# Performance work log

Hardware: AMD Instinct MI355X
Metric: run time of the kernel (lower is better)

The kernel has to match this reference:

```python
import jax, jax.numpy as jnp
import numpy as np
import math


def _align_seq_len(e, target_n):
    # e: (B, H, N_enc, hd) -> (B, H, target_n, hd) via bilinear resize on sqrt grid
    B, H, N_enc, D = e.shape
    if N_enc == target_n:
        return e
    h_e = int(math.sqrt(N_enc))
    h_t = int(math.sqrt(target_n))
    img = jnp.transpose(e, (0, 1, 3, 2)).reshape(B, H, D, h_e, h_e)
    img = jax.image.resize(img, (B, H, D, h_t, h_t), method='bilinear')
    return jnp.transpose(img.reshape(B, H, D, target_n), (0, 1, 3, 2))


def setup_inputs() -> dict:
    key = jax.random.key(0)
    ks = jax.random.split(key, 7)
    B, N, D, H = 4, 1024, 1152, 16
    hd = D // H
    N_enc = 1024
    s_in = 1.0 / math.sqrt(D)
    return {
        'x': jax.random.normal(ks[0], (B, N, D), jnp.float32),
        'enc_k': jax.random.normal(ks[1], (B, H, N_enc, hd), jnp.float32),
        'enc_v': jax.random.normal(ks[2], (B, H, N_enc, hd), jnp.float32),
        'qkv_w': jax.random.normal(ks[3], (3 * D, D), jnp.float32) * s_in,
        'qkv_b': jax.random.normal(ks[4], (3 * D,), jnp.float32) * 0.02,
        'proj_w': jax.random.normal(ks[5], (D, D), jnp.float32) * s_in,
        'proj_b': jax.random.normal(ks[6], (D,), jnp.float32) * 0.02,
        'stage': 2,
    }


def reference(x, enc_k, enc_v, qkv_w, qkv_b, proj_w, proj_b, stage):
    B, N, C = x.shape
    H = enc_k.shape[1]
    hd = C // H
    scale = hd ** (-0.5)

    qkv = (x @ qkv_w.T + qkv_b).reshape(B, N, 3, H, hd)
    qkv = jnp.transpose(qkv, (2, 0, 3, 1, 4))  # (3, B, H, N, hd)
    q, k, v = qkv[0], qkv[1], qkv[2]

    distill_loss = jnp.float32(0.0)
    if stage == 1:
        ek = _align_seq_len(enc_k, N)
        ev = _align_seq_len(enc_v, N)
        attn = jax.nn.softmax(jnp.einsum('bhnd,bhmd->bhnm', q * scale, ek), axis=-1)
        x_out = jnp.einsum('bhnm,bhmd->bhnd', attn, ev)
    elif stage == 2:
        ek = _align_seq_len(enc_k, N)
        ev = _align_seq_len(enc_v, N)
        attn_own = jax.nn.softmax(jnp.einsum('bhnd,bhmd->bhnm', q * scale, k), axis=-1)
        x_out = jnp.einsum('bhnm,bhmd->bhnd', attn_own, v)
        qd = jax.lax.stop_gradient(q)
        attn_enc = jax.nn.softmax(jnp.einsum('bhnd,bhmd->bhnm', qd * scale, ek), axis=-1)
        o_star = jax.lax.stop_gradient(jnp.einsum('bhnm,bhmd->bhnd', attn_enc, ev))
        distill_loss = jnp.mean((x_out - o_star) ** 2)
    else:
        attn = jax.nn.softmax(jnp.einsum('bhnd,bhmd->bhnm', q * scale, k), axis=-1)
        x_out = jnp.einsum('bhnm,bhmd->bhnd', attn, v)

    x_out = jnp.transpose(x_out, (0, 2, 1, 3)).reshape(B, N, C)
    out = x_out @ proj_w.T + proj_b
    return out, distill_loss
```

## Files before the change

### kernel.cpp

```cpp
#include <hip/hip_runtime.h>
#include <hip/hip_bf16.h>

#define PB 4
#define PN 1024
#define PC 1152
#define PH 16
#define PHD 72
#define BH 64
#define QKV_COLS 3456
#define OUT_ELEMS ((size_t)PB*PN*PC)
#define K_DIM 1152

#define CHUNK_HALVES 6144
#define HEAD_HALVES (16*CHUNK_HALVES)
#define BUF_HALVES ((size_t)BH*HEAD_HALVES)

typedef _Float16 half8_t __attribute__((ext_vector_type(8)));
typedef _Float16 half4_t __attribute__((ext_vector_type(4)));
typedef float float4v __attribute__((ext_vector_type(4)));

__device__ __forceinline__ void load16_lds(const _Float16* g, _Float16* l) {
    __builtin_amdgcn_global_load_lds(
        (const __attribute__((address_space(1))) void*)g,
        (__attribute__((address_space(3))) void*)l, 16, 0, 0);
}

__global__ __launch_bounds__(256) void f32_to_f16(
    const float* __restrict__ in, _Float16* __restrict__ out, int n8)
{
    int i = blockIdx.x * 256 + threadIdx.x;
    if (i >= n8) return;
    float4 a = ((const float4*)in)[2 * i];
    float4 b = ((const float4*)in)[2 * i + 1];
    half8_t h;
    h[0] = (_Float16)a.x; h[1] = (_Float16)a.y; h[2] = (_Float16)a.z; h[3] = (_Float16)a.w;
    h[4] = (_Float16)b.x; h[5] = (_Float16)b.y; h[6] = (_Float16)b.z; h[7] = (_Float16)b.w;
    ((half8_t*)out)[i] = h;
}

__global__ __launch_bounds__(256) void zero_qpad(_Float16* __restrict__ qh)
{
    int i = blockIdx.x * 256 + threadIdx.x;
    int chunk = i / 192, within = i - chunk * 192;
    half8_t z = {};
    *(half8_t*)(qh + (size_t)chunk * CHUNK_HALVES + 4608 + within * 8) = z;
}

__global__ __launch_bounds__(256) void enc_convert(
    const float* __restrict__ ek, const float* __restrict__ ev,
    _Float16* __restrict__ ekh, _Float16* __restrict__ evth)
{
    const int bh = blockIdx.y, nblk = blockIdx.x, t = threadIdx.x;
    const float* ksrc = ek + ((size_t)bh * PN + nblk * 64) * PHD;
    const float* vsrc = ev + ((size_t)bh * PN + nblk * 64) * PHD;
    _Float16* kdst = ekh  + ((size_t)bh * 16 + nblk) * CHUNK_HALVES;
    _Float16* vdst = evth + ((size_t)bh * 16 + nblk) * CHUNK_HALVES;
    for (int i = t; i < 64 * 18; i += 256) {
        int n = i / 18, d4 = (i % 18) * 4;
        float4 kv = *(const float4*)&ksrc[n * PHD + d4];
        float4 vv = *(const float4*)&vsrc[n * PHD + d4];
        float ka[4] = {kv.x, kv.y, kv.z, kv.w};
        float va[4] = {vv.x, vv.y, vv.z, vv.w};
#pragma unroll
        for (int kk = 0; kk < 4; ++kk) {
            int d = d4 + kk;
            kdst[(d >> 3) * 512 + n * 8 + (d & 7)] = (_Float16)ka[kk];
            vdst[(n >> 3) * 768 + d * 8 + (n & 7)] = (_Float16)va[kk];
        }
    }
}

template<int MODE>
__global__ __launch_bounds__(256) void gemm_mfma(
    const _Float16* __restrict__ A, const _Float16* __restrict__ Bm,
    const float* __restrict__ bias,
    _Float16* __restrict__ qh, _Float16* __restrict__ kh,
    _Float16* __restrict__ vth, float* __restrict__ out, int c_tiles)
{
    const int t    = threadIdx.x;
    const int lane = t & 63;
    const int w    = t >> 6;
    const int wm   = w >> 1, wn = w & 1;
    const int lrow = lane & 15, quad = lane >> 4;

    const int per_group = c_tiles * 8;
    const int g  = blockIdx.x / per_group;
    const int r_ = blockIdx.x - g * per_group;
    const int m0 = (g * 8 + (r_ & 7)) * 128;
    const int c0 = (r_ >> 3) * 128;

    __shared__ _Float16 As[8192];
    __shared__ _Float16 Bs[8192];

    int rowS[4], koff[4], ldsOff[4];
#pragma unroll
    for (int i = 0; i < 4; ++i) {
        int idx = w * 256 + i * 64 + lane;
        int kt2 = idx >> 9, qq = (idx >> 7) & 3;
        rowS[i]   = idx & 127;
        koff[i]   = kt2 * 32 + qq * 8;
        ldsOff[i] = idx * 8;
    }

    const _Float16* aBase = A  + (size_t)m0 * K_DIM;
    const _Float16* bBase = Bm + (size_t)c0 * K_DIM;

    float4v acc[4][4];
#pragma unroll
    for (int ti = 0; ti < 4; ++ti)
#pragma unroll
        for (int tj = 0; tj < 4; ++tj)
            acc[ti][tj] = (float4v){0.f, 0.f, 0.f, 0.f};

    for (int kb = 0; kb < K_DIM; kb += 64) {
        __syncthreads();
#pragma unroll
        for (int i = 0; i < 4; ++i) {
            load16_lds(aBase + (size_t)rowS[i] * K_DIM + kb + koff[i], &As[ldsOff[i]]);
            load16_lds(bBase + (size_t)rowS[i] * K_DIM + kb + koff[i], &Bs[ldsOff[i]]);
        }
        __syncthreads();
#pragma unroll
        for (int s = 0; s < 2; ++s) {
            half8_t af[4], bf[4];
#pragma unroll
            for (int ti = 0; ti < 4; ++ti)
                af[ti] = *(const half8_t*)&As[(((s * 4 + quad) * 128) + wm * 64 + ti * 16 + lrow) * 8];
#pragma unroll
            for (int tj = 0; tj < 4; ++tj)
                bf[tj] = *(const half8_t*)&Bs[(((s * 4 + quad) * 128) + wn * 64 + tj * 16 + lrow) * 8];
#pragma unroll
            for (int ti = 0; ti < 4; ++ti)
#pragma unroll
                for (int tj = 0; tj < 4; ++tj)
                    acc[ti][tj] = __builtin_amdgcn_mfma_f32_16x16x32_f16(
                        af[ti], bf[tj], acc[ti][tj], 0, 0, 0);
        }
    }

    if (MODE == 0) {
        const float scale = 0.11785113019775792f;
#pragma unroll
        for (int tj = 0; tj < 4; ++tj) {
            int c = c0 + wn * 64 + tj * 16 + lrow;
            float bv = bias[c];
            int jq  = c / PC;
            int rem = c - jq * PC;
            int h   = rem / PHD;
            int d   = rem - h * PHD;
#pragma unroll
            for (int ti = 0; ti < 4; ++ti)
#pragma unroll
                for (int r = 0; r < 4; ++r) {
                    int m = m0 + wm * 64 + ti * 16 + quad * 4 + r;
                    int b = m >> 10, n = m & 1023;
                    int bh = b * PH + h;
                    size_t chunk = ((size_t)bh * 16 + (n >> 6)) * CHUNK_HALVES;
                    float val = acc[ti][tj][r] + bv;
                    if (jq == 0)
                        qh[chunk + (d >> 3) * 512 + (n & 63) * 8 + (d & 7)] = (_Float16)(val * scale);
                    else if (jq == 1)
                        kh[chunk + (d >> 3) * 512 + (n & 63) * 8 + (d & 7)] = (_Float16)val;
                    else
                        vth[chunk + ((n & 63) >> 3) * 768 + d * 8 + (n & 7)] = (_Float16)val;
                }
        }
    } else {
#pragma unroll
        for (int tj = 0; tj < 4; ++tj) {
            int c = c0 + wn * 64 + tj * 16 + lrow;
            float bv = bias[c];
#pragma unroll
            for (int ti = 0; ti < 4; ++ti)
#pragma unroll
                for (int r = 0; r < 4; ++r) {
                    int m = m0 + wm * 64 + ti * 16 + quad * 4 + r;
                    out[(size_t)m * PC + c] = acc[ti][tj][r] + bv;
                }
        }
    }
}

__device__ __forceinline__ void attn_step(
    const _Float16* Qs, const _Float16* Ks, const _Float16* Vts, _Float16* Pw,
    float4v* O, float& m_run, float& l_run, int w, int ln, int quad)
{
    float4v accS[4];
#pragma unroll
    for (int ct = 0; ct < 4; ++ct) accS[ct] = (float4v){0.f, 0.f, 0.f, 0.f};
#pragma unroll
    for (int ks = 0; ks < 3; ++ks) {
        half8_t qf = *(const half8_t*)&Qs[(((ks * 4 + quad) * 64) + w * 16 + ln) * 8];
#pragma unroll
        for (int ct = 0; ct < 4; ++ct) {
            half8_t kf = *(const half8_t*)&Ks[(((ks * 4 + quad) * 64) + ct * 16 + ln) * 8];
            accS[ct] = __builtin_amdgcn_mfma_f32_16x16x32_f16(kf, qf, accS[ct], 0, 0, 0);
        }
    }

    float mx = -1e30f;
#pragma unroll
    for (int ct = 0; ct < 4; ++ct)
#pragma unroll
        for (int r = 0; r < 4; ++r) mx = fmaxf(mx, accS[ct][r]);
    mx = fmaxf(mx, __shfl_xor(mx, 16));
    mx = fmaxf(mx, __shfl_xor(mx, 32));
    float m_new = fmaxf(m_run, mx);
    float alpha = __expf(m_run - m_new);
    m_run = m_new;

    float lsum = 0.f;
    const int pbase = (quad >> 1) * 128 + ln * 8 + (quad & 1) * 4;
#pragma unroll
    for (int ct = 0; ct < 4; ++ct) {
        half4_t pk;
#pragma unroll
        for (int r = 0; r < 4; ++r) {
            float p = __expf(accS[ct][r] - m_new);
            lsum += p;
            pk[r] = (_Float16)p;
        }
        *(half4_t*)&Pw[pbase + ct * 256] = pk;
    }
    lsum += __shfl_xor(lsum, 16);
    lsum += __shfl_xor(lsum, 32);
    l_run = l_run * alpha + lsum;

#pragma unroll
    for (int ct = 0; ct < 5; ++ct) O[ct] *= alpha;

#pragma unroll
    for (int ks = 0; ks < 2; ++ks) {
        half8_t pf = *(const half8_t*)&Pw[(ks * 4 + quad) * 128 + ln * 8];
#pragma unroll
        for (int ct = 0; ct < 5; ++ct) {
            half8_t vf = *(const half8_t*)&Vts[(((ks * 4 + quad) * 96) + ct * 16 + ln) * 8];
            O[ct] = __builtin_amdgcn_mfma_f32_16x16x32_f16(vf, pf, O[ct], 0, 0, 0);
        }
    }
}

__global__ __launch_bounds__(256) void attn_fused(
    const _Float16* __restrict__ qh, const _Float16* __restrict__ kh,
    const _Float16* __restrict__ vth,
    const _Float16* __restrict__ ekh, const _Float16* __restrict__ evth,
    _Float16* __restrict__ xouth, float* __restrict__ loss_out)
{
    const int t = threadIdx.x;
    const int lane = t & 63;
    const int w = t >> 6;
    const int ln = lane & 15;
    const int quad = lane >> 4;

    const int lid  = blockIdx.x;
    const int bh   = (lid & 7) * 8 + ((lid >> 3) >> 4);
    const int nblk = (lid >> 3) & 15;

    __shared__ _Float16 Qs[CHUNK_HALVES];
    __shared__ _Float16 KsA[CHUNK_HALVES];
    __shared__ _Float16 VsA[CHUNK_HALVES];
    __shared__ _Float16 KsB[CHUNK_HALVES];
    __shared__ _Float16 VsB[CHUNK_HALVES];
    __shared__ _Float16 Ps[4096];
    __shared__ float red[256];

    _Float16* Pw = Ps + w * 1024;

    const _Float16* qc = qh + ((size_t)bh * 16 + nblk) * CHUNK_HALVES;
    const _Float16* kbo = kh   + (size_t)bh * HEAD_HALVES;
    const _Float16* vbo = vth  + (size_t)bh * HEAD_HALVES;
    const _Float16* kbe = ekh  + (size_t)bh * HEAD_HALVES;
    const _Float16* vbe = evth + (size_t)bh * HEAD_HALVES;

#pragma unroll
    for (int i = 0; i < 3; ++i) {
        int u = i * 256 + t;
        load16_lds(qc + u * 8, &Qs[u * 8]);
        load16_lds(kbo + u * 8, &KsA[u * 8]);
        load16_lds(vbo + u * 8, &VsA[u * 8]);
    }
    __syncthreads();

    float4v Oo[5], Oe[5];
#pragma unroll
    for (int ct = 0; ct < 5; ++ct) {
        Oo[ct] = (float4v){0.f, 0.f, 0.f, 0.f};
        Oe[ct] = (float4v){0.f, 0.f, 0.f, 0.f};
    }
    float m_o = -1e30f, l_o = 0.f;
    float m_e = -1e30f, l_e = 0.f;

    for (int kt = 0; kt < 16; ++kt) {
        {
            const _Float16* kc = kbe + (size_t)kt * CHUNK_HALVES;
            const _Float16* vc = vbe + (size_t)kt * CHUNK_HALVES;
#pragma unroll
            for (int i = 0; i < 3; ++i) {
                int u = i * 256 + t;
                load16_lds(kc + u * 8, &KsB[u * 8]);
                load16_lds(vc + u * 8, &VsB[u * 8]);
            }
        }
        attn_step(Qs, KsA, VsA, Pw, Oo, m_o, l_o, w, ln, quad);
        __syncthreads();

        if (kt < 15) {
            const _Float16* kc = kbo + (size_t)(kt + 1) * CHUNK_HALVES;
            const _Float16* vc = vbo + (size_t)(kt + 1) * CHUNK_HALVES;
#pragma unroll
            for (int i = 0; i < 3; ++i) {
                int u = i * 256 + t;
                load16_lds(kc + u * 8, &KsA[u * 8]);
                load16_lds(vc + u * 8, &VsA[u * 8]);
            }
        }
        attn_step(Qs, KsB, VsB, Pw, Oe, m_e, l_e, w, ln, quad);
        __syncthreads();
    }

    const float inv_o = 1.0f / l_o;
    const float inv_e = 1.0f / l_e;

    const int b = bh >> 4, h = bh & 15;
    const int nrow = nblk * 64 + w * 16 + ln;

    float lacc = 0.f;
    const size_t rowbase = (size_t)(b * PN + nrow) * PC + h * PHD;
#pragma unroll
    for (int ct = 0; ct < 5; ++ct) {
        int d0 = ct * 16 + quad * 4;
        if (d0 < PHD) {
            half4_t oh;
#pragma unroll
            for (int r = 0; r < 4; ++r) {
                float own = Oo[ct][r] * inv_o;
                oh[r] = (_Float16)own;
                float df = own - Oe[ct][r] * inv_e;
                lacc += df * df;
            }
            *(half4_t*)&xouth[rowbase + d0] = oh;
        }
    }

    red[t] = lacc;
    __syncthreads();
    for (int off = 128; off > 0; off >>= 1) {
        if (t < off) red[t] += red[t + off];
        __syncthreads();
    }
    if (t == 0) atomicAdd(loss_out, red[0] * (1.0f / (float)OUT_ELEMS));
}

extern "C" void kernel_launch(void* const* d_in, const int* in_sizes, int n_in,
                              void* d_out, int out_size, void* d_ws, size_t ws_size,
                              hipStream_t stream)
{
    const float* x      = (const float*)d_in[0];
    const float* enc_k  = (const float*)d_in[1];
    const float* enc_v  = (const float*)d_in[2];
    const float* qkv_w  = (const float*)d_in[3];
    const float* qkv_b  = (const float*)d_in[4];
    const float* proj_w = (const float*)d_in[5];
    const float* proj_b = (const float*)d_in[6];

    float* out = (float*)d_out;

    _Float16* x_h     = (_Float16*)d_ws;
    _Float16* qkvw_h  = x_h + OUT_ELEMS;
    _Float16* projw_h = qkvw_h + (size_t)QKV_COLS * PC;
    _Float16* xout_h  = projw_h + (size_t)PC * PC;
    _Float16* q_h     = xout_h + OUT_ELEMS;
    _Float16* k_h     = q_h  + BUF_HALVES;
    _Float16* vt_h    = k_h  + BUF_HALVES;
    _Float16* ek_h    = vt_h + BUF_HALVES;
    _Float16* evt_h   = ek_h + BUF_HALVES;

    const int n8_x  = (int)(OUT_ELEMS / 8);
    const int n8_qw = QKV_COLS * PC / 8;
    const int n8_pw = PC * PC / 8;

    hipMemsetAsync(out + OUT_ELEMS, 0, sizeof(float), stream);
    zero_qpad<<<768, 256, 0, stream>>>(q_h);

    f32_to_f16<<<(n8_x  + 255) / 256, 256, 0, stream>>>(x,      x_h,     n8_x);
    f32_to_f16<<<(n8_qw + 255) / 256, 256, 0, stream>>>(qkv_w,  qkvw_h,  n8_qw);
    f32_to_f16<<<(n8_pw + 255) / 256, 256, 0, stream>>>(proj_w, projw_h, n8_pw);
    enc_convert<<<dim3(16, BH), 256, 0, stream>>>(enc_k, enc_v, ek_h, evt_h);

    gemm_mfma<0><<<(QKV_COLS / 128) * ((PB * PN) / 128), 256, 0, stream>>>(
        x_h, qkvw_h, qkv_b, q_h, k_h, vt_h, nullptr, QKV_COLS / 128);

    attn_fused<<<16 * BH, 256, 0, stream>>>(
        q_h, k_h, vt_h, ek_h, evt_h, xout_h, out + OUT_ELEMS);

    gemm_mfma<1><<<(PC / 128) * ((PB * PN) / 128), 256, 0, stream>>>(
        xout_h, projw_h, proj_b, nullptr, nullptr, nullptr, out, PC / 128);
}
```

Measured before the change: 356.7 us.

## Shrink attention LDS footprint, keep Q in registers, vectorize GEMM epilogue stores

The attention kernel drops the Q tile and the double-buffered K/V tiles from LDS. It now loads Q fragments into registers once, uses a single K/V buffer, and runs the own-attention and encoder-attention passes one after the other. It also sets launch bounds asking for more resident blocks per CU. This buys occupancy but gives up the load/compute overlap the double buffering provided. Separately, the GEMM swaps MFMA operands for Q/K/out tiles so each lane holds contiguous columns, writes the epilogue with half4/float4 vector stores, and folds log2(e) into the Q scale so softmax can use exp2f.

```diff
diff --git a/kernel.cpp b/kernel.cpp
--- a/kernel.cpp
+++ b/kernel.cpp
@@ -18,6 +18,8 @@
 typedef _Float16 half8_t __attribute__((ext_vector_type(8)));
 typedef _Float16 half4_t __attribute__((ext_vector_type(4)));
 typedef float float4v __attribute__((ext_vector_type(4)));
+
+#define QSCALE (0.11785113019775792f * 1.4426950408889634f)
 
 __device__ __forceinline__ void load16_lds(const _Float16* g, _Float16* l) {
     __builtin_amdgcn_global_load_lds(
@@ -89,6 +91,8 @@
     const int m0 = (g * 8 + (r_ & 7)) * 128;
     const int c0 = (r_ >> 3) * 128;
 
+    const bool tr = (MODE == 1) || (c0 < 2 * PC);
+
     __shared__ _Float16 As[8192];
     __shared__ _Float16 Bs[8192];
 
@@ -129,72 +133,97 @@
 #pragma unroll
             for (int tj = 0; tj < 4; ++tj)
                 bf[tj] = *(const half8_t*)&Bs[(((s * 4 + quad) * 128) + wn * 64 + tj * 16 + lrow) * 8];
-#pragma unroll
-            for (int ti = 0; ti < 4; ++ti)
-#pragma unroll
-                for (int tj = 0; tj < 4; ++tj)
-                    acc[ti][tj] = __builtin_amdgcn_mfma_f32_16x16x32_f16(
-                        af[ti], bf[tj], acc[ti][tj], 0, 0, 0);
-        }
-    }
-
-    if (MODE == 0) {
-        const float scale = 0.11785113019775792f;
+            if (tr) {
+#pragma unroll
+                for (int ti = 0; ti < 4; ++ti)
+#pragma unroll
+                    for (int tj = 0; tj < 4; ++tj)
+                        acc[ti][tj] = __builtin_amdgcn_mfma_f32_16x16x32_f16(
+                            bf[tj], af[ti], acc[ti][tj], 0, 0, 0);
+            } else {
+#pragma unroll
+                for (int ti = 0; ti < 4; ++ti)
+#pragma unroll
+                    for (int tj = 0; tj < 4; ++tj)
+                        acc[ti][tj] = __builtin_amdgcn_mfma_f32_16x16x32_f16(
+                            af[ti], bf[tj], acc[ti][tj], 0, 0, 0);
+            }
+        }
+    }
+
+    if (MODE == 1) {
 #pragma unroll
         for (int tj = 0; tj < 4; ++tj) {
-            int c = c0 + wn * 64 + tj * 16 + lrow;
-            float bv = bias[c];
-            int jq  = c / PC;
-            int rem = c - jq * PC;
+            int cg = c0 + wn * 64 + tj * 16 + quad * 4;
+            float4v bv = *(const float4v*)&bias[cg];
+#pragma unroll
+            for (int ti = 0; ti < 4; ++ti) {
+                int m = m0 + wm * 64 + ti * 16 + lrow;
+                float4v o;
+#pragma unroll
+                for (int r = 0; r < 4; ++r) o[r] = acc[ti][tj][r] + bv[r];
+                *(float4v*)&out[(size_t)m * PC + cg] = o;
+            }
+        }
+    } else if (tr) {
+        const int jq = c0 / PC;
+        const float mulv = (jq == 0) ? QSCALE : 1.f;
+        _Float16* dstp = (jq == 0) ? qh : kh;
+#pragma unroll
+        for (int tj = 0; tj < 4; ++tj) {
+            int cg  = c0 + wn * 64 + tj * 16 + quad * 4;
+            int rem = cg - jq * PC;
+            int h   = rem / PHD;
+            int ds  = rem - h * PHD;
+            float4v bv = *(const float4v*)&bias[cg];
+#pragma unroll
+            for (int ti = 0; ti < 4; ++ti) {
+                int m = m0 + wm * 64 + ti * 16 + lrow;
+                int b = m >> 10, n = m & 1023;
+                size_t chunk = ((size_t)(b * PH + h) * 16 + (n >> 6)) * CHUNK_HALVES;
+                half4_t hv;
+#pragma unroll
+                for (int r = 0; r < 4; ++r)
+                    hv[r] = (_Float16)((acc[ti][tj][r] + bv[r]) * mulv);
+                *(half4_t*)&dstp[chunk + (ds >> 3) * 512 + (n & 63) * 8 + (ds & 7)] = hv;
+            }
+        }
+    } else {
+#pragma unroll
+        for (int tj = 0; tj < 4; ++tj) {
+            int c   = c0 + wn * 64 + tj * 16 + lrow;
+            int rem = c - 2 * PC;
             int h   = rem / PHD;
             int d   = rem - h * PHD;
-#pragma unroll
-            for (int ti = 0; ti < 4; ++ti)
-#pragma unroll
-                for (int r = 0; r < 4; ++r) {
-                    int m = m0 + wm * 64 + ti * 16 + quad * 4 + r;
-                    int b = m >> 10, n = m & 1023;
-                    int bh = b * PH + h;
-                    size_t chunk = ((size_t)bh * 16 + (n >> 6)) * CHUNK_HALVES;
-                    float val = acc[ti][tj][r] + bv;
-                    if (jq == 0)
-                        qh[chunk + (d >> 3) * 512 + (n & 63) * 8 + (d & 7)] = (_Float16)(val * scale);
-                    else if (jq == 1)
-                        kh[chunk + (d >> 3) * 512 + (n & 63) * 8 + (d & 7)] = (_Float16)val;
-                    else
-                        vth[chunk + ((n & 63) >> 3) * 768 + d * 8 + (n & 7)] = (_Float16)val;
-                }
-        }
-    } else {
-#pragma unroll
-        for (int tj = 0; tj < 4; ++tj) {
-            int c = c0 + wn * 64 + tj * 16 + lrow;
             float bv = bias[c];
 #pragma unroll
-            for (int ti = 0; ti < 4; ++ti)
-#pragma unroll
-                for (int r = 0; r < 4; ++r) {
-                    int m = m0 + wm * 64 + ti * 16 + quad * 4 + r;
-                    out[(size_t)m * PC + c] = acc[ti][tj][r] + bv;
-                }
+            for (int ti = 0; ti < 4; ++ti) {
+                int mg = m0 + wm * 64 + ti * 16 + quad * 4;
+                int b = mg >> 10, n = mg & 1023;
+                size_t chunk = ((size_t)(b * PH + h) * 16 + (n >> 6)) * CHUNK_HALVES;
+                half4_t hv;
+#pragma unroll
+                for (int r = 0; r < 4; ++r)
+                    hv[r] = (_Float16)(acc[ti][tj][r] + bv);
+                *(half4_t*)&vth[chunk + ((n & 63) >> 3) * 768 + d * 8 + (n & 7)] = hv;
+            }
         }
     }
 }
 
 __device__ __forceinline__ void attn_step(
-    const _Float16* Qs, const _Float16* Ks, const _Float16* Vts, _Float16* Pw,
-    float4v* O, float& m_run, float& l_run, int w, int ln, int quad)
+    const half8_t* qf, const _Float16* Ks, const _Float16* Vts, _Float16* Pw,
+    float4v* O, float& m_run, float& l_run, int ln, int quad)
 {
     float4v accS[4];
 #pragma unroll
     for (int ct = 0; ct < 4; ++ct) accS[ct] = (float4v){0.f, 0.f, 0.f, 0.f};
 #pragma unroll
     for (int ks = 0; ks < 3; ++ks) {
-        half8_t qf = *(const half8_t*)&Qs[(((ks * 4 + quad) * 64) + w * 16 + ln) * 8];
 #pragma unroll
         for (int ct = 0; ct < 4; ++ct) {
             half8_t kf = *(const half8_t*)&Ks[(((ks * 4 + quad) * 64) + ct * 16 + ln) * 8];
-            accS[ct] = __builtin_amdgcn_mfma_f32_16x16x32_f16(kf, qf, accS[ct], 0, 0, 0);
+            accS[ct] = __builtin_amdgcn_mfma_f32_16x16x32_f16(kf, qf[ks], accS[ct], 0, 0, 0);
         }
     }
 
@@ -206,7 +235,7 @@
     mx = fmaxf(mx, __shfl_xor(mx, 16));
     mx = fmaxf(mx, __shfl_xor(mx, 32));
     float m_new = fmaxf(m_run, mx);
-    float alpha = __expf(m_run - m_new);
+    float alpha = exp2f(m_run - m_new);
     m_run = m_new;
 
     float lsum = 0.f;
@@ -216,7 +245,7 @@
         half4_t pk;
 #pragma unroll
         for (int r = 0; r < 4; ++r) {
-            float p = __expf(accS[ct][r] - m_new);
+            float p = exp2f(accS[ct][r] - m_new);
             lsum += p;
             pk[r] = (_Float16)p;
         }
@@ -240,7 +269,7 @@
     }
 }
 
-__global__ __launch_bounds__(256) void attn_fused(
+__global__ __launch_bounds__(256, 4) void attn_fused(
     const _Float16* __restrict__ qh, const _Float16* __restrict__ kh,
     const _Float16* __restrict__ vth,
     const _Float16* __restrict__ ekh, const _Float16* __restrict__ evth,
@@ -256,31 +285,24 @@
     const int bh   = (lid & 7) * 8 + ((lid >> 3) >> 4);
     const int nblk = (lid >> 3) & 15;
 
-    __shared__ _Float16 Qs[CHUNK_HALVES];
-    __shared__ _Float16 KsA[CHUNK_HALVES];
-    __shared__ _Float16 VsA[CHUNK_HALVES];
-    __shared__ _Float16 KsB[CHUNK_HALVES];
-    __shared__ _Float16 VsB[CHUNK_HALVES];
+    __shared__ _Float16 Ks[CHUNK_HALVES];
+    __shared__ _Float16 Vs[CHUNK_HALVES];
     __shared__ _Float16 Ps[4096];
     __shared__ float red[256];
 
     _Float16* Pw = Ps + w * 1024;
 
     const _Float16* qc = qh + ((size_t)bh * 16 + nblk) * CHUNK_HALVES;
+    half8_t qf[3];
+#pragma unroll
+    for (int ks = 0; ks < 3; ++ks)
+        qf[ks] = *(const half8_t*)&qc[(((ks * 4 + quad) * 64) + w * 16 + ln) * 8];
+
     const _Float16* kbo = kh   + (size_t)bh * HEAD_HALVES;
     const _Float16* vbo = vth  + (size_t)bh * HEAD_HALVES;
     const _Float16* kbe = ekh  + (size_t)bh * HEAD_HALVES;
     const _Float16* vbe = evth + (size_t)bh * HEAD_HALVES;
 
-#pragma unroll
-    for (int i = 0; i < 3; ++i) {
-        int u = i * 256 + t;
-        load16_lds(qc + u * 8, &Qs[u * 8]);
-        load16_lds(kbo + u * 8, &KsA[u * 8]);
-        load16_lds(vbo + u * 8, &VsA[u * 8]);
-    }
-    __syncthreads();
-
     float4v Oo[5], Oe[5];
 #pragma unroll
     for (int ct = 0; ct < 5; ++ct) {
@@ -291,31 +313,30 @@
     float m_e = -1e30f, l_e = 0.f;
 
     for (int kt = 0; kt < 16; ++kt) {
-        {
-            const _Float16* kc = kbe + (size_t)kt * CHUNK_HALVES;
-            const _Float16* vc = vbe + (size_t)kt * CHUNK_HALVES;
-#pragma unroll
-            for (int i = 0; i < 3; ++i) {
-                int u = i * 256 + t;
-                load16_lds(kc + u * 8, &KsB[u * 8]);
-                load16_lds(vc + u * 8, &VsB[u * 8]);
-            }
-        }
-        attn_step(Qs, KsA, VsA, Pw, Oo, m_o, l_o, w, ln, quad);
-        __syncthreads();
-
-        if (kt < 15) {
-            const _Float16* kc = kbo + (size_t)(kt + 1) * CHUNK_HALVES;
-            const _Float16* vc = vbo + (size_t)(kt + 1) * CHUNK_HALVES;
-#pragma unroll
-            for (int i = 0; i < 3; ++i) {
-                int u = i * 256 + t;
-                load16_lds(kc + u * 8, &KsA[u * 8]);
-                load16_lds(vc + u * 8, &VsA[u * 8]);
-            }
-        }
-        attn_step(Qs, KsB, VsB, Pw, Oe, m_e, l_e, w, ln, quad);
-        __syncthreads();
+        const _Float16* kc = kbo + (size_t)kt * CHUNK_HALVES;
+        const _Float16* vc = vbo + (size_t)kt * CHUNK_HALVES;
+        __syncthreads();
+#pragma unroll
+        for (int i = 0; i < 3; ++i) {
+            int u = i * 256 + t;
+            load16_lds(kc + u * 8, &Ks[u * 8]);
+            load16_lds(vc + u * 8, &Vs[u * 8]);
+        }
+        __syncthreads();
+        attn_step(qf, Ks, Vs, Pw, Oo, m_o, l_o, ln, quad);
+    }
+    for (int kt = 0; kt < 16; ++kt) {
+        const _Float16* kc = kbe + (size_t)kt * CHUNK_HALVES;
+        const _Float16* vc = vbe + (size_t)kt * CHUNK_HALVES;
+        __syncthreads();
+#pragma unroll
+        for (int i = 0; i < 3; ++i) {
+            int u = i * 256 + t;
+            load16_lds(kc + u * 8, &Ks[u * 8]);
+            load16_lds(vc + u * 8, &Vs[u * 8]);
+        }
+        __syncthreads();
+        attn_step(qf, Ks, Vs, Pw, Oe, m_e, l_e, ln, quad);
     }
 
     const float inv_o = 1.0f / l_o;
```

Result: faster. 342.8 us (-3.9%).
